# Kernel tuning notes

Hardware: AMD Instinct MI355X
Metric: run time of the kernel (lower is better)

## Reference

```python
import jax, jax.numpy as jnp
import numpy as np

NEG = -9e15


def make_adj_mask(edge_index, n):
    # dense mask: 0 on edges and diagonal, -9e15 elsewhere (vectorized version of the source loop)
    A = jnp.full((n, n), NEG, dtype=jnp.float32)
    A = jnp.where(jnp.eye(n, dtype=bool), 0.0, A)
    A = A.at[edge_index[0], edge_index[1]].set(0.0)
    return A


def gat_layer(x, W, b, a_left, a_right, mask, num_heads, concat, alpha=0.2):
    n = x.shape[0]
    feats = (x @ W + b).reshape(n, num_heads, -1)           # [n, h, c]
    s_src = jnp.einsum('nhc,ch->nh', feats, a_left)          # score of source (column) node
    s_tgt = jnp.einsum('nhc,ch->nh', feats, a_right)         # score of target (row) node
    # all_scores[i, j, h] = s_src[j, h] + s_tgt[i, h]
    scores = jax.nn.leaky_relu(s_src[None, :, :] + s_tgt[:, None, :], alpha)
    scores = jnp.transpose(scores, (2, 0, 1)) + mask         # [h, n, n]
    attn = jax.nn.softmax(scores, axis=2)
    out = jnp.einsum('hij,jhc->ihc', attn, feats)            # [n, h, c]
    if concat:
        return out.reshape(n, -1)
    return out.mean(axis=1)


def setup_inputs() -> dict:
    key = jax.random.key(0)
    ks = jax.random.split(key, 10)
    N, F, H, C_HID, N_CLS, E = 4096, 512, 8, 64, 7, 65536
    c_ph = C_HID // H  # 8 per head
    s = 0.05
    return {
        'x': jax.random.normal(ks[0], (N, F), dtype=jnp.float32),
        'edge_index': jax.random.randint(ks[1], (2, E), 0, N, dtype=jnp.int32),
        'W1': jax.random.normal(ks[2], (F, C_HID), dtype=jnp.float32) * s,
        'b1': jnp.zeros((C_HID,), dtype=jnp.float32),
        'a_left1': jax.random.normal(ks[3], (c_ph, H), dtype=jnp.float32) * s,
        'a_right1': jax.random.normal(ks[4], (c_ph, H), dtype=jnp.float32) * s,
        'W2': jax.random.normal(ks[5], (C_HID, N_CLS), dtype=jnp.float32) * s,
        'b2': jnp.zeros((N_CLS,), dtype=jnp.float32),
        'a_left2': jax.random.normal(ks[6], (N_CLS, 1), dtype=jnp.float32) * s,
        'a_right2': jax.random.normal(ks[7], (N_CLS, 1), dtype=jnp.float32) * s,
    }


def reference(x, edge_index, W1, b1, a_left1, a_right1, W2, b2, a_left2, a_right2):
    n = x.shape[0]
    mask = make_adj_mask(edge_index, n)
    h1 = gat_layer(x, W1, b1, a_left1, a_right1, mask, num_heads=8, concat=True)
    h1 = jax.nn.elu(h1)
    out = gat_layer(h1, W2, b2, a_left2, a_right2, mask, num_heads=1, concat=False)
    return out
```

## Files before the change

kernel.cpp:

```cpp
#include <hip/hip_runtime.h>
#include <math.h>

#define NNODES 4096
#define WPR 128
#define FDIM 512
#define CHID 64
#define NHEAD 8
#define NCLS 7
#define MAXD 4096

typedef short bf16x8 __attribute__((ext_vector_type(8)));
typedef float f32x4  __attribute__((ext_vector_type(4)));

static __device__ inline short f2bf(float f) {
    union { float f; unsigned u; } v; v.f = f;
    unsigned r = v.u + 0x7fffu + ((v.u >> 16) & 1u);
    return (short)(r >> 16);
}

__global__ void k_init(unsigned int* __restrict__ adj, int* __restrict__ deg,
                       const float* __restrict__ W1, short* __restrict__ Bp) {
    const int gid = blockIdx.x * 256 + threadIdx.x;
    const int gs = gridDim.x * 256;
    for (int t = gid; t < NNODES * WPR; t += gs) adj[t] = 0u;
    for (int t = gid; t < NNODES; t += gs) deg[t] = 0;
    for (int t = gid; t < 32768; t += gs) {
        int j = t & 7, l = (t >> 3) & 63, cq = (t >> 9) & 3, kb = t >> 11;
        Bp[t] = f2bf(W1[(kb * 32 + (l >> 4) * 8 + j) * 64 + (cq * 16 + (l & 15))]);
    }
}

__global__ void k_scatter(const int* __restrict__ ei, int E, unsigned int* __restrict__ adj,
                          int* __restrict__ deg, int* __restrict__ nbrL) {
    const int t = blockIdx.x * 256 + threadIdx.x;
    if (t >= E + NNODES) return;
    int r, c;
    if (t < E) { r = ei[t]; c = ei[E + t]; }
    else       { r = c = t - E; }
    const unsigned bit = 1u << (c & 31);
    const unsigned old = atomicOr(&adj[r * WPR + (c >> 5)], bit);
    if (!(old & bit)) {
        const int p = atomicAdd(&deg[r], 1);
        nbrL[r * MAXD + p] = c;
    }
}

__global__ void __launch_bounds__(256) k_gemm(const float* __restrict__ x, const short* __restrict__ Bp,
                                              const float* __restrict__ b1, const float* __restrict__ al,
                                              const float* __restrict__ ar,
                                              float* __restrict__ feats, float* __restrict__ s1) {
    __shared__ float red[4][4][64][4];
    const int w = threadIdx.x >> 6, l = threadIdx.x & 63;
    const int row0 = blockIdx.x * 16;
    const int arow = row0 + (l & 15);
    const int koff = (l >> 4) * 8;
    const bf16x8* bp = (const bf16x8*)Bp;
    f32x4 acc0 = {0,0,0,0}, acc1 = {0,0,0,0}, acc2 = {0,0,0,0}, acc3 = {0,0,0,0};
    #pragma unroll
    for (int q = 0; q < 4; ++q) {
        const int kb = w * 4 + q;
        const float* ap = &x[arow * FDIM + kb * 32 + koff];
        const float4 a0 = *(const float4*)ap;
        const float4 a1 = *(const float4*)(ap + 4);
        bf16x8 af = { f2bf(a0.x), f2bf(a0.y), f2bf(a0.z), f2bf(a0.w),
                      f2bf(a1.x), f2bf(a1.y), f2bf(a1.z), f2bf(a1.w) };
        acc0 = __builtin_amdgcn_mfma_f32_16x16x32_bf16(af, bp[(kb * 4 + 0) * 64 + l], acc0, 0, 0, 0);
        acc1 = __builtin_amdgcn_mfma_f32_16x16x32_bf16(af, bp[(kb * 4 + 1) * 64 + l], acc1, 0, 0, 0);
        acc2 = __builtin_amdgcn_mfma_f32_16x16x32_bf16(af, bp[(kb * 4 + 2) * 64 + l], acc2, 0, 0, 0);
        acc3 = __builtin_amdgcn_mfma_f32_16x16x32_bf16(af, bp[(kb * 4 + 3) * 64 + l], acc3, 0, 0, 0);
    }
    #pragma unroll
    for (int r = 0; r < 4; ++r) {
        red[w][0][l][r] = acc0[r];
        red[w][1][l][r] = acc1[r];
        red[w][2][l][r] = acc2[r];
        red[w][3][l][r] = acc3[r];
    }
    __syncthreads();
    const int col = w * 16 + (l & 15);
    const int r0 = row0 + (l >> 4) * 4;
    const float bias = b1[col];
    const int c = col & 7, h = col >> 3;
    const float vl = al[c * NHEAD + h];
    const float vr = ar[c * NHEAD + h];
    #pragma unroll
    for (int r = 0; r < 4; ++r) {
        float fv = red[0][w][l][r] + red[1][w][l][r] + red[2][w][l][r] + red[3][w][l][r] + bias;
        feats[(r0 + r) * CHID + col] = fv;
        float ps = fv * vl, pt = fv * vr;
        ps += __shfl_xor(ps, 1); ps += __shfl_xor(ps, 2); ps += __shfl_xor(ps, 4);
        pt += __shfl_xor(pt, 1); pt += __shfl_xor(pt, 2); pt += __shfl_xor(pt, 4);
        if ((l & 7) == 0) {
            s1[(r0 + r) * 16 + h] = ps;
            s1[(r0 + r) * 16 + 8 + h] = pt;
        }
    }
}

__global__ void __launch_bounds__(256) k_attn1(const int* __restrict__ nbrL, const int* __restrict__ deg,
                                               const float* __restrict__ feats,
                                               const float* __restrict__ s1,
                                               const float* __restrict__ W2,
                                               const float* __restrict__ b2,
                                               const float* __restrict__ al2,
                                               const float* __restrict__ ar2,
                                               float* __restrict__ feats2,
                                               float* __restrict__ s2) {
    const int w = threadIdx.x >> 6, l = threadIdx.x & 63;
    const int i = blockIdx.x * 4 + w;
    const int h = l >> 3;
    const int nn = deg[i];
    const float stgt = s1[i * 16 + 8 + h];
    float den = 0.f, acc = 0.f;
    if (nn <= 64) {
        const int jv = nbrL[i * MAXD + (l < nn ? l : 0)];
        for (int k = 0; k < nn; ++k) {
            const int j = __shfl(jv, k);
            float sc = s1[j * 16 + h] + stgt;
            sc = sc > 0.f ? sc : 0.2f * sc;
            const float p = __expf(sc);
            den += p;
            acc = fmaf(p, feats[j * CHID + l], acc);
        }
    } else {
        for (int k0 = 0; k0 < nn; k0 += 64) {
            const int rem = nn - k0;
            const int cmax = rem < 64 ? rem : 64;
            const int jv = nbrL[i * MAXD + k0 + (l < cmax ? l : 0)];
            for (int k = 0; k < cmax; ++k) {
                const int j = __shfl(jv, k);
                float sc = s1[j * 16 + h] + stgt;
                sc = sc > 0.f ? sc : 0.2f * sc;
                const float p = __expf(sc);
                den += p;
                acc = fmaf(p, feats[j * CHID + l], acc);
            }
        }
    }
    const float o = acc / den;
    const float h1v = o > 0.f ? o : (__expf(o) - 1.f);
    float t7[NCLS];
    #pragma unroll
    for (int c2 = 0; c2 < NCLS; ++c2) {
        float p = h1v * W2[l * NCLS + c2];
        p += __shfl_xor(p, 1);  p += __shfl_xor(p, 2);  p += __shfl_xor(p, 4);
        p += __shfl_xor(p, 8);  p += __shfl_xor(p, 16); p += __shfl_xor(p, 32);
        t7[c2] = p + b2[c2];
    }
    if (l == 0) {
        float ss = 0.f, st = 0.f;
        #pragma unroll
        for (int c2 = 0; c2 < NCLS; ++c2) {
            ss = fmaf(t7[c2], al2[c2], ss);
            st = fmaf(t7[c2], ar2[c2], st);
        }
        #pragma unroll
        for (int c2 = 0; c2 < NCLS; ++c2) feats2[i * 8 + c2] = t7[c2];
        feats2[i * 8 + 7] = 0.f;
        s2[i * 2] = ss;
        s2[i * 2 + 1] = st;
    }
}

__global__ void __launch_bounds__(256) k_attn2(const int* __restrict__ nbrL, const int* __restrict__ deg,
                                               const float* __restrict__ feats2,
                                               const float* __restrict__ s2,
                                               float* __restrict__ out) {
    const int w = threadIdx.x >> 6, l = threadIdx.x & 63;
    const int i = blockIdx.x * 4 + w;
    const int nn = deg[i];
    const int c = l & 7;
    const float stgt = s2[i * 2 + 1];
    float den = 0.f, acc = 0.f;
    if (nn <= 64) {
        const int jv = nbrL[i * MAXD + (l < nn ? l : 0)];
        for (int k = 0; k < nn; ++k) {
            const int j = __shfl(jv, k);
            float sc = s2[j * 2] + stgt;
            sc = sc > 0.f ? sc : 0.2f * sc;
            const float p = __expf(sc);
            den += p;
            acc = fmaf(p, feats2[j * 8 + c], acc);
        }
    } else {
        for (int k0 = 0; k0 < nn; k0 += 64) {
            const int rem = nn - k0;
            const int cmax = rem < 64 ? rem : 64;
            const int jv = nbrL[i * MAXD + k0 + (l < cmax ? l : 0)];
            for (int k = 0; k < cmax; ++k) {
                const int j = __shfl(jv, k);
                float sc = s2[j * 2] + stgt;
                sc = sc > 0.f ? sc : 0.2f * sc;
                const float p = __expf(sc);
                den += p;
                acc = fmaf(p, feats2[j * 8 + c], acc);
            }
        }
    }
    if (l < NCLS) out[i * NCLS + l] = acc / den;
}

extern "C" void kernel_launch(void* const* d_in, const int* in_sizes, int n_in,
                              void* d_out, int out_size, void* d_ws, size_t ws_size,
                              hipStream_t stream) {
    const float* x   = (const float*)d_in[0];
    const int*   ei  = (const int*)d_in[1];
    const float* W1  = (const float*)d_in[2];
    const float* b1  = (const float*)d_in[3];
    const float* al1 = (const float*)d_in[4];
    const float* ar1 = (const float*)d_in[5];
    const float* W2  = (const float*)d_in[6];
    const float* b2  = (const float*)d_in[7];
    const float* al2 = (const float*)d_in[8];
    const float* ar2 = (const float*)d_in[9];
    float* out = (float*)d_out;
    int E = in_sizes[1] / 2;

    char* ws = (char*)d_ws;
    unsigned int* adj = (unsigned int*)ws;
    short* Bp     = (short*)(ws + (2u << 20));
    float* feats1 = (float*)(ws + (3u << 20));
    float* s1     = (float*)(ws + (4u << 20));
    float* feats2 = (float*)(ws + (5u << 20));
    float* s2     = (float*)(ws + (6u << 20));
    int*   deg    = (int*)  (ws + (7u << 20));
    int*   nbrL   = (int*)  (ws + (16u << 20));

    k_init   <<<2048, 256, 0, stream>>>(adj, deg, W1, Bp);
    k_scatter<<<(E + NNODES + 255) / 256, 256, 0, stream>>>(ei, E, adj, deg, nbrL);
    k_gemm   <<<NNODES / 16, 256, 0, stream>>>(x, Bp, b1, al1, ar1, feats1, s1);
    k_attn1  <<<NNODES / 4, 256, 0, stream>>>(nbrL, deg, feats1, s1, W2, b2, al2, ar2, feats2, s2);
    k_attn2  <<<NNODES / 4, 256, 0, stream>>>(nbrL, deg, feats2, s2, out);
}
```

Before: 110.5 us.

## Fuse edge scatter into GEMM kernel and dedupe neighbors at attention time

Drops the dense adjacency bitmap and its zeroing pass. The edge scatter now runs in extra blocks of the GEMM launch, and W1 is converted to bf16 inside the GEMM instead of in a separate prepack pass. Duplicate edges are no longer filtered with atomicOr at scatter time. The attention kernels skip repeated neighbor indices using a ballot compare, or a wave-wide scan in the high-degree path. This cuts two launches and a 2 MB memset, but adds per-neighbor dedup work and quadratic scans when a node has many neighbors.

```diff
diff --git a/kernel.cpp b/kernel.cpp
--- a/kernel.cpp
+++ b/kernel.cpp
@@ -2,7 +2,6 @@
 #include <math.h>
 
 #define NNODES 4096
-#define WPR 128
 #define FDIM 512
 #define CHID 64
 #define NHEAD 8
@@ -18,43 +17,31 @@
     return (short)(r >> 16);
 }
 
-__global__ void k_init(unsigned int* __restrict__ adj, int* __restrict__ deg,
-                       const float* __restrict__ W1, short* __restrict__ Bp) {
-    const int gid = blockIdx.x * 256 + threadIdx.x;
-    const int gs = gridDim.x * 256;
-    for (int t = gid; t < NNODES * WPR; t += gs) adj[t] = 0u;
-    for (int t = gid; t < NNODES; t += gs) deg[t] = 0;
-    for (int t = gid; t < 32768; t += gs) {
-        int j = t & 7, l = (t >> 3) & 63, cq = (t >> 9) & 3, kb = t >> 11;
-        Bp[t] = f2bf(W1[(kb * 32 + (l >> 4) * 8 + j) * 64 + (cq * 16 + (l & 15))]);
-    }
-}
-
-__global__ void k_scatter(const int* __restrict__ ei, int E, unsigned int* __restrict__ adj,
-                          int* __restrict__ deg, int* __restrict__ nbrL) {
-    const int t = blockIdx.x * 256 + threadIdx.x;
-    if (t >= E + NNODES) return;
-    int r, c;
-    if (t < E) { r = ei[t]; c = ei[E + t]; }
-    else       { r = c = t - E; }
-    const unsigned bit = 1u << (c & 31);
-    const unsigned old = atomicOr(&adj[r * WPR + (c >> 5)], bit);
-    if (!(old & bit)) {
-        const int p = atomicAdd(&deg[r], 1);
-        nbrL[r * MAXD + p] = c;
-    }
-}
-
-__global__ void __launch_bounds__(256) k_gemm(const float* __restrict__ x, const short* __restrict__ Bp,
+__global__ void k_zero(int* __restrict__ deg) {
+    deg[blockIdx.x * 256 + threadIdx.x] = 0;
+}
+
+__global__ void __launch_bounds__(256) k_main(const float* __restrict__ x, const float* __restrict__ W1,
                                               const float* __restrict__ b1, const float* __restrict__ al,
-                                              const float* __restrict__ ar,
-                                              float* __restrict__ feats, float* __restrict__ s1) {
+                                              const float* __restrict__ ar, const int* __restrict__ ei,
+                                              int E, float* __restrict__ feats, float* __restrict__ s1,
+                                              int* __restrict__ deg, int* __restrict__ nbrL) {
+    if (blockIdx.x >= 256) {
+        const int t = (blockIdx.x - 256) * 256 + threadIdx.x;
+        if (t < E + NNODES) {
+            int r, c;
+            if (t < E) { r = ei[t]; c = ei[E + t]; }
+            else       { r = c = t - E; }
+            const int p = atomicAdd(&deg[r], 1);
+            if (p < MAXD) nbrL[r * MAXD + p] = c;
+        }
+        return;
+    }
     __shared__ float red[4][4][64][4];
     const int w = threadIdx.x >> 6, l = threadIdx.x & 63;
     const int row0 = blockIdx.x * 16;
     const int arow = row0 + (l & 15);
     const int koff = (l >> 4) * 8;
-    const bf16x8* bp = (const bf16x8*)Bp;
     f32x4 acc0 = {0,0,0,0}, acc1 = {0,0,0,0}, acc2 = {0,0,0,0}, acc3 = {0,0,0,0};
     #pragma unroll
     for (int q = 0; q < 4; ++q) {
@@ -64,10 +51,19 @@
         const float4 a1 = *(const float4*)(ap + 4);
         bf16x8 af = { f2bf(a0.x), f2bf(a0.y), f2bf(a0.z), f2bf(a0.w),
                       f2bf(a1.x), f2bf(a1.y), f2bf(a1.z), f2bf(a1.w) };
-        acc0 = __builtin_amdgcn_mfma_f32_16x16x32_bf16(af, bp[(kb * 4 + 0) * 64 + l], acc0, 0, 0, 0);
-        acc1 = __builtin_amdgcn_mfma_f32_16x16x32_bf16(af, bp[(kb * 4 + 1) * 64 + l], acc1, 0, 0, 0);
-        acc2 = __builtin_amdgcn_mfma_f32_16x16x32_bf16(af, bp[(kb * 4 + 2) * 64 + l], acc2, 0, 0, 0);
-        acc3 = __builtin_amdgcn_mfma_f32_16x16x32_bf16(af, bp[(kb * 4 + 3) * 64 + l], acc3, 0, 0, 0);
+        const float* wp = &W1[(kb * 32 + (l >> 4) * 8) * 64 + (l & 15)];
+        bf16x8 bf0, bf1, bf2, bf3;
+        #pragma unroll
+        for (int j = 0; j < 8; ++j) {
+            bf0[j] = f2bf(wp[j * 64 + 0]);
+            bf1[j] = f2bf(wp[j * 64 + 16]);
+            bf2[j] = f2bf(wp[j * 64 + 32]);
+            bf3[j] = f2bf(wp[j * 64 + 48]);
+        }
+        acc0 = __builtin_amdgcn_mfma_f32_16x16x32_bf16(af, bf0, acc0, 0, 0, 0);
+        acc1 = __builtin_amdgcn_mfma_f32_16x16x32_bf16(af, bf1, acc1, 0, 0, 0);
+        acc2 = __builtin_amdgcn_mfma_f32_16x16x32_bf16(af, bf2, acc2, 0, 0, 0);
+        acc3 = __builtin_amdgcn_mfma_f32_16x16x32_bf16(af, bf3, acc3, 0, 0, 0);
     }
     #pragma unroll
     for (int r = 0; r < 4; ++r) {
@@ -109,13 +105,15 @@
     const int w = threadIdx.x >> 6, l = threadIdx.x & 63;
     const int i = blockIdx.x * 4 + w;
     const int h = l >> 3;
-    const int nn = deg[i];
+    int nn = deg[i]; if (nn > MAXD) nn = MAXD;
     const float stgt = s1[i * 16 + 8 + h];
     float den = 0.f, acc = 0.f;
     if (nn <= 64) {
-        const int jv = nbrL[i * MAXD + (l < nn ? l : 0)];
+        const int jv = (l < nn) ? nbrL[i * MAXD + l] : (0x40000000 + l);
         for (int k = 0; k < nn; ++k) {
             const int j = __shfl(jv, k);
+            const unsigned long long eq = __ballot(jv == j);
+            if (eq & ((1ULL << k) - 1ULL)) continue;
             float sc = s1[j * 16 + h] + stgt;
             sc = sc > 0.f ? sc : 0.2f * sc;
             const float p = __expf(sc);
@@ -123,18 +121,17 @@
             acc = fmaf(p, feats[j * CHID + l], acc);
         }
     } else {
-        for (int k0 = 0; k0 < nn; k0 += 64) {
-            const int rem = nn - k0;
-            const int cmax = rem < 64 ? rem : 64;
-            const int jv = nbrL[i * MAXD + k0 + (l < cmax ? l : 0)];
-            for (int k = 0; k < cmax; ++k) {
-                const int j = __shfl(jv, k);
-                float sc = s1[j * 16 + h] + stgt;
-                sc = sc > 0.f ? sc : 0.2f * sc;
-                const float p = __expf(sc);
-                den += p;
-                acc = fmaf(p, feats[j * CHID + l], acc);
-            }
+        const int base = i * MAXD;
+        for (int k = 0; k < nn; ++k) {
+            const int j = nbrL[base + k];
+            bool d = false;
+            for (int kk = l; kk < k; kk += 64) d |= (nbrL[base + kk] == j);
+            if (__any(d)) continue;
+            float sc = s1[j * 16 + h] + stgt;
+            sc = sc > 0.f ? sc : 0.2f * sc;
+            const float p = __expf(sc);
+            den += p;
+            acc = fmaf(p, feats[j * CHID + l], acc);
         }
     }
     const float o = acc / den;
@@ -168,14 +165,16 @@
                                                float* __restrict__ out) {
     const int w = threadIdx.x >> 6, l = threadIdx.x & 63;
     const int i = blockIdx.x * 4 + w;
-    const int nn = deg[i];
+    int nn = deg[i]; if (nn > MAXD) nn = MAXD;
     const int c = l & 7;
     const float stgt = s2[i * 2 + 1];
     float den = 0.f, acc = 0.f;
     if (nn <= 64) {
-        const int jv = nbrL[i * MAXD + (l < nn ? l : 0)];
+        const int jv = (l < nn) ? nbrL[i * MAXD + l] : (0x40000000 + l);
         for (int k = 0; k < nn; ++k) {
             const int j = __shfl(jv, k);
+            const unsigned long long eq = __ballot(jv == j);
+            if (eq & ((1ULL << k) - 1ULL)) continue;
             float sc = s2[j * 2] + stgt;
             sc = sc > 0.f ? sc : 0.2f * sc;
             const float p = __expf(sc);
@@ -183,18 +182,17 @@
             acc = fmaf(p, feats2[j * 8 + c], acc);
         }
     } else {
-        for (int k0 = 0; k0 < nn; k0 += 64) {
-            const int rem = nn - k0;
-            const int cmax = rem < 64 ? rem : 64;
-            const int jv = nbrL[i * MAXD + k0 + (l < cmax ? l : 0)];
-            for (int k = 0; k < cmax; ++k) {
-                const int j = __shfl(jv, k);
-                float sc = s2[j * 2] + stgt;
-                sc = sc > 0.f ? sc : 0.2f * sc;
-                const float p = __expf(sc);
-                den += p;
-                acc = fmaf(p, feats2[j * 8 + c], acc);
-            }
+        const int base = i * MAXD;
+        for (int k = 0; k < nn; ++k) {
+            const int j = nbrL[base + k];
+            bool d = false;
+            for (int kk = l; kk < k; kk += 64) d |= (nbrL[base + kk] == j);
+            if (__any(d)) continue;
+            float sc = s2[j * 2] + stgt;
+            sc = sc > 0.f ? sc : 0.2f * sc;
+            const float p = __expf(sc);
+            den += p;
+            acc = fmaf(p, feats2[j * 8 + c], acc);
         }
     }
     if (l < NCLS) out[i * NCLS + l] = acc / den;
@@ -217,18 +215,16 @@
     int E = in_sizes[1] / 2;
 
     char* ws = (char*)d_ws;
-    unsigned int* adj = (unsigned int*)ws;
-    short* Bp     = (short*)(ws + (2u << 20));
-    float* feats1 = (float*)(ws + (3u << 20));
-    float* s1     = (float*)(ws + (4u << 20));
-    float* feats2 = (float*)(ws + (5u << 20));
-    float* s2     = (float*)(ws + (6u << 20));
-    int*   deg    = (int*)  (ws + (7u << 20));
-    int*   nbrL   = (int*)  (ws + (16u << 20));
-
-    k_init   <<<2048, 256, 0, stream>>>(adj, deg, W1, Bp);
-    k_scatter<<<(E + NNODES + 255) / 256, 256, 0, stream>>>(ei, E, adj, deg, nbrL);
-    k_gemm   <<<NNODES / 16, 256, 0, stream>>>(x, Bp, b1, al1, ar1, feats1, s1);
+    float* feats1 = (float*)(ws);
+    float* s1     = (float*)(ws + (1u << 20));
+    float* feats2 = (float*)(ws + (2u << 20));
+    float* s2     = (float*)(ws + (3u << 20));
+    int*   deg    = (int*)  (ws + (4u << 20));
+    int*   nbrL   = (int*)  (ws + (8u << 20));
+
+    const int scat_blocks = (E + NNODES + 255) / 256;
+    k_zero   <<<NNODES / 256, 256, 0, stream>>>(deg);
+    k_main   <<<256 + scat_blocks, 256, 0, stream>>>(x, W1, b1, al1, ar1, ei, E, feats1, s1, deg, nbrL);
     k_attn1  <<<NNODES / 4, 256, 0, stream>>>(nbrL, deg, feats1, s1, W2, b2, al2, ar2, feats2, s2);
     k_attn2  <<<NNODES / 4, 256, 0, stream>>>(nbrL, deg, feats2, s2, out);
 }
```

New measurement: 108.1 us. -2.2%, faster.
